# Optimization experiments

Hardware: AMD Instinct MI355X
Metric: run time of the kernel (lower is better)

## Reference

```python
import jax, jax.numpy as jnp
import numpy as np
from jax.scipy.special import gammaln

EPS = 1e-20
EULER_GAMMA = 0.5772156649015329
B, L, D, H, DK, DV = 8, 512, 1024, 16, 64, 64
K_WEIBULL = 0.5
BETA_GAMMA = 1.0
SCALE = 1.0 / np.sqrt(DK)  # torch code DIVIDES by this -> multiply by sqrt(DK)


def setup_inputs() -> dict:
    key = jax.random.key(0)
    ks = jax.random.split(key, 20)
    f = jnp.float32
    return {
        "queries": jax.random.normal(ks[0], (B, L, D), f),
        "keys": jax.random.normal(ks[1], (B, L, D), f),
        "values": jax.random.normal(ks[2], (B, L, D), f),
        "unif": jax.random.uniform(ks[3], (B, H, L, L), f),
        "Wq": jax.random.normal(ks[4], (D, H * DK), f) * 0.03,
        "bq": jnp.zeros((H * DK,), f),
        "Wk": jax.random.normal(ks[5], (D, H * DK), f) * 0.03,
        "bk": jnp.zeros((H * DK,), f),
        "Wv": jax.random.normal(ks[6], (D, H * DV), f) * 0.03,
        "bv": jnp.zeros((H * DV,), f),
        "Wo": jax.random.normal(ks[7], (H * DV, D), f) * 0.03,
        "bo": jnp.zeros((D,), f),
        "Wp1": jax.random.normal(ks[8], (DK, D), f) * 0.05,
        "bp1": jnp.zeros((D,), f),
        "Wp2": jax.random.normal(ks[9], (D, 1), f) * 0.05,
        "bp2": jnp.zeros((1,), f),
    }


def reference(queries, keys, values, unif, Wq, bq, Wk, bk, Wv, bv, Wo, bo, Wp1, bp1, Wp2, bp2):
    # projections -> multi-head layout
    q = (queries @ Wq + bq).reshape(B, L, H, DK).transpose(0, 2, 1, 3)   # [B,H,Q,dk]
    k = (keys @ Wk + bk).reshape(B, L, H, DK).transpose(0, 2, 1, 3)     # [B,H,K,dk]
    v = (values @ Wv + bv).reshape(B, L, H, DV).transpose(0, 2, 1, 3)   # [B,H,K,dv]

    # faithful: torch divides by scale=1/sqrt(dk)
    att = jnp.einsum("bhqd,bhkd->bhqk", q, k) / SCALE                   # [B,H,Q,K]

    # prior MLP on keys (per key position)
    h = (k @ Wp1 + bp1)                                                  # [B,H,K,D]
    h = jnp.where(h >= 0, h, 0.01 * h)                                   # LeakyReLU
    dot_gamma = (h @ Wp2 + bp2).transpose(0, 1, 3, 2)                    # [B,H,1,K]
    prior_w = jax.nn.softmax(dot_gamma, axis=-1)
    alpha = prior_w * BETA_GAMMA                                         # [B,H,1,K]

    # Weibull reparameterized stochastic attention
    inv_k = 1.0 / K_WEIBULL
    logprobs = jnp.log(jax.nn.softmax(att, axis=-1) + EPS)
    gumbel_w = jnp.log(-jnp.log(1.0 - unif + EPS) + EPS)
    att_s = jax.nn.softmax(logprobs - gammaln(1.0 + inv_k + inv_k * gumbel_w), axis=-1)

    lg1 = gammaln(jnp.float32(1.0 + inv_k))
    kl = -(alpha * (logprobs - lg1)
           - EULER_GAMMA * alpha * inv_k
           - BETA_GAMMA * jnp.exp(logprobs - lg1 + lg1)
           + alpha * jnp.log(BETA_GAMMA + EPS)
           - gammaln(alpha + EPS))
    kl_mean = kl.mean()

    out = jnp.einsum("bhqk,bhkd->bhqd", att_s, v)                        # [B,H,Q,dv]
    out = out.transpose(0, 2, 1, 3).reshape(B, L, H * DV)
    out = out @ Wo + bo                                                  # [B,Q,D]
    return out, kl_mean
```

## Files before the change

### kernel.cpp

```cpp
#include <hip/hip_runtime.h>
#include <math.h>


typedef __bf16 bh_t;
typedef bh_t  bh8  __attribute__((ext_vector_type(8)));
typedef float f32x4 __attribute__((ext_vector_type(4)));
typedef _Float16 hf_t;
typedef hf_t  hf4  __attribute__((ext_vector_type(4)));

#define MFMA_BF16 __builtin_amdgcn_mfma_f32_16x16x32_bf16

static constexpr size_t P2 = 4096ull*1024ull*2ull;
static constexpr size_t W2 = 1024ull*1024ull*2ull;
static constexpr size_t O_QHI = 0;
static constexpr size_t O_QLO = O_QHI + P2;
static constexpr size_t O_KHI = O_QLO + P2;
static constexpr size_t O_KLO = O_KHI + P2;
static constexpr size_t O_VT  = O_KLO + P2;
static constexpr size_t O_WQH = O_VT  + P2;
static constexpr size_t O_WQL = O_WQH + W2;
static constexpr size_t O_WKH = O_WQL + W2;
static constexpr size_t O_WKL = O_WKH + W2;
static constexpr size_t O_WVH = O_WKL + W2;
static constexpr size_t O_WVL = O_WVH + W2;
static constexpr size_t O_WOH = O_WVL + W2;
static constexpr size_t O_WOL = O_WOH + W2;
static constexpr size_t O_WP1H = O_WOL + W2;
static constexpr size_t O_WP1L = O_WP1H + 1024ull*64ull*2ull;
static constexpr size_t O_DG   = O_WP1L + 1024ull*64ull*2ull;
static constexpr size_t O_ALPHA= O_DG + 65536ull*4ull;
static constexpr size_t O_HO   = O_ALPHA + 65536ull*4ull;
static constexpr size_t O_GS   = O_HO + P2;
static constexpr size_t O_ACC  = O_GS + 512ull*65536ull*2ull;
static constexpr size_t WS_TOTAL = O_ACC + 256;

__device__ __align__(256) unsigned char g_ws[WS_TOTAL];

__device__ __forceinline__ float lgamma_fast(float x)
{
    float ax = (x < 0.5f) ? (1.0f - x) : x;
    float p  = ax*(ax+1.f)*(ax+2.f)*(ax+3.f);
    bool  sm = ax < 4.0f;
    float lsh = sm ? __logf(p) : 0.0f;
    float y   = sm ? (ax + 4.0f) : ax;
    float ly  = __logf(y);
    float inv = __builtin_amdgcn_rcpf(y);
    float i2  = inv * inv;
    float stir = fmaf(y - 0.5f, ly, -y) + 0.91893853320467274f
               + inv * fmaf(-2.7777777777e-3f, i2, 8.3333333333e-2f);
    float core = stir - lsh;
    float r  = x - rintf(x);
    float sp = __sinf(3.14159265358979f * r);
    float rres = 1.14472988584940017f - __logf(fabsf(sp)) - core;
    return (x < 0.5f) ? rres : core;
}

__global__ void k_zero(double* a)
{
    if (threadIdx.x < 4) a[threadIdx.x] = 0.0;
}

__global__ __launch_bounds__(256) void k_transpose_split(
    const float* __restrict__ in, bh_t* __restrict__ oh, bh_t* __restrict__ ol,
    int rows, int cols)
{
    __shared__ float tile[64][65];
    const int bc = blockIdx.x * 64, br = blockIdx.y * 64;
    const int t = threadIdx.x;
    const int r = t >> 2, c0 = (t & 3) * 16;
#pragma unroll
    for (int i = 0; i < 16; i += 4) {
        float4 v = *(const float4*)(in + (size_t)(br + r) * cols + bc + c0 + i);
        tile[r][c0+i]   = v.x; tile[r][c0+i+1] = v.y;
        tile[r][c0+i+2] = v.z; tile[r][c0+i+3] = v.w;
    }
    __syncthreads();
    bh8 hv[2], lv[2];
#pragma unroll
    for (int i = 0; i < 16; i++) {
        float x = tile[c0 + i][r];
        bh_t hh = (bh_t)x;
        hv[i >> 3][i & 7] = hh;
        lv[i >> 3][i & 7] = (bh_t)(x - (float)hh);
    }
    size_t ob = (size_t)(bc + r) * rows + br + c0;
    *(bh8*)(oh + ob)     = hv[0];
    *(bh8*)(oh + ob + 8) = hv[1];
    *(bh8*)(ol + ob)     = lv[0];
    *(bh8*)(ol + ob + 8) = lv[1];
}

__global__ __launch_bounds__(256) void k_transpose_split4(
    const float* __restrict__ W0, const float* __restrict__ W1,
    const float* __restrict__ W2_, const float* __restrict__ W3,
    bh_t* __restrict__ OH)
{
    __shared__ float tile[64][65];
    const int z = blockIdx.z;
    const float* in = (z == 0) ? W0 : (z == 1) ? W1 : (z == 2) ? W2_ : W3;
    bh_t* oh = OH + (size_t)z * 2ull * 1024ull * 1024ull;
    bh_t* ol = oh + 1024ull * 1024ull;
    const int bc = blockIdx.x * 64, br = blockIdx.y * 64;
    const int t = threadIdx.x;
    const int r = t >> 2, c0 = (t & 3) * 16;
#pragma unroll
    for (int i = 0; i < 16; i += 4) {
        float4 v = *(const float4*)(in + (size_t)(br + r) * 1024 + bc + c0 + i);
        tile[r][c0+i]   = v.x; tile[r][c0+i+1] = v.y;
        tile[r][c0+i+2] = v.z; tile[r][c0+i+3] = v.w;
    }
    __syncthreads();
    bh8 hv[2], lv[2];
#pragma unroll
    for (int i = 0; i < 16; i++) {
        float x = tile[c0 + i][r];
        bh_t hh = (bh_t)x;
        hv[i >> 3][i & 7] = hh;
        lv[i >> 3][i & 7] = (bh_t)(x - (float)hh);
    }
    size_t ob = (size_t)(bc + r) * 1024 + br + c0;
    *(bh8*)(oh + ob)     = hv[0];
    *(bh8*)(oh + ob + 8) = hv[1];
    *(bh8*)(ol + ob)     = lv[0];
    *(bh8*)(ol + ob + 8) = lv[1];
}

template<bool SPLIT, int OMODE, bool ABF>
__global__ __launch_bounds__(256) void k_gemm(
    const float* __restrict__ A, const bh_t* __restrict__ ABH,
    const bh_t* __restrict__ WH, const bh_t* __restrict__ WL,
    const float* __restrict__ bias,
    bh_t* __restrict__ oh, bh_t* __restrict__ ol, float* __restrict__ of)
{
    __shared__ __align__(16) bh_t Ah[64][40];
    __shared__ __align__(16) bh_t Al[64][40];
    __shared__ __align__(16) bh_t Bh[64][40];
    __shared__ __align__(16) bh_t Bl[64][40];
    const int n0 = blockIdx.x * 64, m0 = blockIdx.y * 64;
    const int t = threadIdx.x;
    const int lane = t & 63, w = t >> 6;
    const int lr = lane & 15, kg = lane >> 4;
    const int wm = (w & 1) * 32, wn = (w >> 1) * 32;
    const int ar = t >> 2, ac = (t & 3) * 8;
    f32x4 acc[2][2] = {};

    for (int kt = 0; kt < 1024; kt += 32) {
        __syncthreads();
        {
            if constexpr (ABF) {
                *(bh8*)&Ah[ar][ac] = *(const bh8*)(ABH + (size_t)(m0 + ar) * 1024 + kt + ac);
            } else {
                const float* ap = A + (size_t)(m0 + ar) * 1024 + kt + ac;
                float4 v0 = *(const float4*)ap;
                float4 v1 = *(const float4*)(ap + 4);
                float xs[8] = {v0.x, v0.y, v0.z, v0.w, v1.x, v1.y, v1.z, v1.w};
                bh8 h, l;
#pragma unroll
                for (int i = 0; i < 8; i++) {
                    bh_t hh = (bh_t)xs[i];
                    h[i] = hh;
                    l[i] = (bh_t)(xs[i] - (float)hh);
                }
                *(bh8*)&Ah[ar][ac] = h;
                if constexpr (SPLIT) *(bh8*)&Al[ar][ac] = l;
            }
            size_t wb = (size_t)(n0 + ar) * 1024 + kt + ac;
            *(bh8*)&Bh[ar][ac] = *(const bh8*)(WH + wb);
            if constexpr (SPLIT) *(bh8*)&Bl[ar][ac] = *(const bh8*)(WL + wb);
        }
        __syncthreads();
#pragma unroll
        for (int fm = 0; fm < 2; fm++) {
            bh8 a_h = *(bh8*)&Ah[wm + fm*16 + lr][kg * 8];
#pragma unroll
            for (int fn = 0; fn < 2; fn++) {
                bh8 b_h = *(bh8*)&Bh[wn + fn*16 + lr][kg * 8];
                acc[fm][fn] = MFMA_BF16(a_h, b_h, acc[fm][fn], 0, 0, 0);
                if constexpr (SPLIT) {
                    bh8 a_l = *(bh8*)&Al[wm + fm*16 + lr][kg * 8];
                    bh8 b_l = *(bh8*)&Bl[wn + fn*16 + lr][kg * 8];
                    acc[fm][fn] = MFMA_BF16(a_h, b_l, acc[fm][fn], 0, 0, 0);
                    acc[fm][fn] = MFMA_BF16(a_l, b_h, acc[fm][fn], 0, 0, 0);
                }
            }
        }
    }
#pragma unroll
    for (int fm = 0; fm < 2; fm++)
#pragma unroll
    for (int fn = 0; fn < 2; fn++) {
        int col = n0 + wn + fn*16 + lr;
        float bv = bias[col];
#pragma unroll
        for (int r = 0; r < 4; r++) {
            int row = m0 + wm + fm*16 + kg*4 + r;
            float c = acc[fm][fn][r] + bv;
            size_t idx = (size_t)row * 1024 + col;
            if constexpr (OMODE == 0) {
                bh_t hh = (bh_t)c;
                oh[idx] = hh;
                ol[idx] = (bh_t)(c - (float)hh);
            } else if constexpr (OMODE == 1) {
                oh[idx] = (bh_t)c;
            } else if constexpr (OMODE == 2) {
                of[idx] = c;
            } else {
                int bb = row >> 9, ll = row & 511;
                oh[(((size_t)(bb*16 + (col >> 6)) * 64) + (col & 63)) * 512 + ll] = (bh_t)c;
            }
        }
    }
}

__global__ __launch_bounds__(256) void k_prior(
    const bh_t* __restrict__ KH, const bh_t* __restrict__ WP1T,
    const float* __restrict__ bp1, const float* __restrict__ wp2,
    const float* __restrict__ bp2, float* __restrict__ DG)
{
    __shared__ __align__(16) bh_t Kt[64][72];
    __shared__ __align__(16) bh_t Wt[64][72];
    const int lt = blockIdx.x, h = blockIdx.y, b = blockIdx.z;
    const int t = threadIdx.x, lane = t & 63, w = t >> 6;
    const int lr = lane & 15, kg = lane >> 4;
    {
        int r = t >> 2, j0 = (t & 3) * 16;
        const bh_t* src = KH + ((size_t)(b*512 + lt*64 + r)) * 1024 + h*64 + j0;
        *(bh8*)&Kt[r][j0]     = *(const bh8*)src;
        *(bh8*)&Kt[r][j0 + 8] = *(const bh8*)(src + 8);
    }
    __syncthreads();
    bh8 af0 = *(bh8*)&Kt[w*16 + lr][kg * 8];
    bh8 af1 = *(bh8*)&Kt[w*16 + lr][32 + kg * 8];
    float dgp[4] = {0.f, 0.f, 0.f, 0.f};
    for (int dt = 0; dt < 16; dt++) {
        __syncthreads();
        {
            int r = t >> 2, j0 = (t & 3) * 16;
            const bh_t* src = WP1T + (size_t)(dt*64 + r) * 64 + j0;
            *(bh8*)&Wt[r][j0]     = *(const bh8*)src;
            *(bh8*)&Wt[r][j0 + 8] = *(const bh8*)(src + 8);
        }
        __syncthreads();
#pragma unroll
        for (int fn = 0; fn < 4; fn++) {
            bh8 b0 = *(bh8*)&Wt[fn*16 + lr][kg * 8];
            bh8 b1 = *(bh8*)&Wt[fn*16 + lr][32 + kg * 8];
            f32x4 acc = {};
            acc = MFMA_BF16(af0, b0, acc, 0, 0, 0);
            acc = MFMA_BF16(af1, b1, acc, 0, 0, 0);
            int d = dt*64 + fn*16 + lr;
            float bpv = bp1[d], wvv = wp2[d];
#pragma unroll
            for (int r = 0; r < 4; r++) {
                float hv = acc[r] + bpv;
                hv = (hv >= 0.f) ? hv : 0.01f * hv;
                dgp[r] = fmaf(hv, wvv, dgp[r]);
            }
        }
    }
#pragma unroll
    for (int r = 0; r < 4; r++) {
        float v = dgp[r];
        v += __shfl_xor(v, 1); v += __shfl_xor(v, 2);
        v += __shfl_xor(v, 4); v += __shfl_xor(v, 8);
        dgp[r] = v;
    }
    if (lr == 0) {
        float b2 = bp2[0];
        int bh = b * 16 + h;
#pragma unroll
        for (int r = 0; r < 4; r++)
            DG[(size_t)bh*512 + lt*64 + w*16 + kg*4 + r] = dgp[r] + b2;
    }
}

__global__ __launch_bounds__(512) void k_alpha(
    const float* __restrict__ DG, float* __restrict__ AL, double* __restrict__ acc)
{
    __shared__ float red[512];
    const int bh = blockIdx.x, t = threadIdx.x;
    float v = DG[(size_t)bh * 512 + t];
    red[t] = v; __syncthreads();
    for (int s = 256; s > 0; s >>= 1) { if (t < s) red[t] = fmaxf(red[t], red[t+s]); __syncthreads(); }
    float m = red[0]; __syncthreads();
    float e = expf(v - m);
    red[t] = e; __syncthreads();
    for (int s = 256; s > 0; s >>= 1) { if (t < s) red[t] += red[t+s]; __syncthreads(); }
    float ssum = red[0]; __syncthreads();
    float a = e / ssum;
    AL[(size_t)bh * 512 + t] = a;
    float t2 = a * 1.8475785103630112f + lgammaf(a + 1e-20f);
    red[t] = t2; __syncthreads();
    for (int s = 256; s > 0; s >>= 1) { if (t < s) red[t] += red[t+s]; __syncthreads(); }
    if (t == 0) atomicAdd(&acc[2], (double)red[0]);
}

__global__ __launch_bounds__(512, 3) void k_attn(
    const bh_t* __restrict__ QH, const bh_t* __restrict__ QL,
    const bh_t* __restrict__ KH, const bh_t* __restrict__ KL,
    const bh_t* __restrict__ VT, const float* __restrict__ U,
    const float* __restrict__ AL, bh_t* __restrict__ HOB,
    hf_t* __restrict__ GS, double* __restrict__ acc)
{
    __shared__ __align__(16) bh_t KtH[64][72];
    __shared__ __align__(16) bh_t KtL[64][72];
    __shared__ __align__(16) bh_t Vt[64][72];
    __shared__ __align__(16) bh_t Sl[8][16][72];
    __shared__ float Asm[64];
    __shared__ float red[512];

    const int flat = blockIdx.x;
    const int bh = flat & 127, qc = flat >> 7;
    const int b = bh >> 4, h = bh & 15;
    const int t = threadIdx.x, w = t >> 6, lane = t & 63;
    const int lr = lane & 15, kg = lane >> 4;
    const int q0 = qc * 128 + w * 16;
    const int sr = t >> 3, sj = (t & 7) * 8;
    const float* Up = U + ((size_t)bh * 512 + q0 + kg * 4) * 512;
    hf_t* GSp = GS + (size_t)flat * 65536 + (size_t)w * 8192;

    bh8 qh[2], ql[2];
    {
        size_t qb = ((size_t)(b * 512) + q0 + lr) * 1024 + h * 64;
        qh[0] = *(const bh8*)(QH + qb + kg * 8);
        qh[1] = *(const bh8*)(QH + qb + 32 + kg * 8);
        ql[0] = *(const bh8*)(QL + qb + kg * 8);
        ql[1] = *(const bh8*)(QL + qb + 32 + kg * 8);
    }
    float C[4];

    {
        float M1[4], Z1[4];
#pragma unroll
        for (int r = 0; r < 4; r++) { M1[r] = -INFINITY; Z1[r] = 0.f; }

        for (int kt = 0; kt < 8; kt++) {
            __syncthreads();
            {
                size_t src = ((size_t)(b*512 + kt*64 + sr)) * 1024 + h*64 + sj;
                *(bh8*)&KtH[sr][sj] = *(const bh8*)(KH + src);
                *(bh8*)&KtL[sr][sj] = *(const bh8*)(KL + src);
            }
            __syncthreads();
            f32x4 av[4];
#pragma unroll
            for (int fn = 0; fn < 4; fn++) {
                f32x4 a = {};
#pragma unroll
                for (int ks = 0; ks < 2; ks++) {
                    bh8 kb  = *(bh8*)&KtH[fn*16 + lr][ks*32 + kg*8];
                    bh8 kl2 = *(bh8*)&KtL[fn*16 + lr][ks*32 + kg*8];
                    a = MFMA_BF16(qh[ks], kb,  a, 0, 0, 0);
                    a = MFMA_BF16(qh[ks], kl2, a, 0, 0, 0);
                    a = MFMA_BF16(ql[ks], kb,  a, 0, 0, 0);
                }
#pragma unroll
                for (int r = 0; r < 4; r++) a[r] *= 8.0f;
                av[fn] = a;
                int k = kt * 64 + fn * 16 + lr;
                hf4 gh;
#pragma unroll
                for (int r = 0; r < 4; r++) {
                    float u  = Up[(size_t)r * 512 + k];
                    float tt = (1.0f - u) + 1e-20f;
                    float gl = 1e-20f - __logf(tt);
                    float g  = __logf(gl);
                    gh[r] = (hf_t)lgamma_fast(fmaf(2.0f, g, 3.0f));
                }
                *(hf4*)(GSp + ((size_t)(kt*4 + fn) * 64 + lane) * 4) = gh;
            }
#pragma unroll
            for (int r = 0; r < 4; r++) {
                float mx = fmaxf(fmaxf(av[0][r], av[1][r]), fmaxf(av[2][r], av[3][r]));
                mx = fmaxf(mx, __shfl_xor(mx, 1));
                mx = fmaxf(mx, __shfl_xor(mx, 2));
                mx = fmaxf(mx, __shfl_xor(mx, 4));
                mx = fmaxf(mx, __shfl_xor(mx, 8));
                float nm = fmaxf(M1[r], mx);
                float es = __expf(av[0][r]-nm) + __expf(av[1][r]-nm)
                         + __expf(av[2][r]-nm) + __expf(av[3][r]-nm);
                es += __shfl_xor(es, 1); es += __shfl_xor(es, 2);
                es += __shfl_xor(es, 4); es += __shfl_xor(es, 8);
                Z1[r] = Z1[r] * __expf(M1[r] - nm) + es;
                M1[r] = nm;
            }
        }
#pragma unroll
        for (int r = 0; r < 4; r++) C[r] = M1[r] + logf(Z1[r]);
    }

    float M2[4], Z2[4];
    f32x4 oacc[4] = {};
#pragma unroll
    for (int r = 0; r < 4; r++) { M2[r] = -INFINITY; Z2[r] = 0.f; }
    float S1f = 0.f;

    for (int kt = 0; kt < 8; kt++) {
        __syncthreads();
        {
            size_t src = ((size_t)(b*512 + kt*64 + sr)) * 1024 + h*64 + sj;
            *(bh8*)&KtH[sr][sj] = *(const bh8*)(KH + src);
            *(bh8*)&KtL[sr][sj] = *(const bh8*)(KL + src);
            const bh_t* vsrc = VT + ((size_t)bh * 64 + sr) * 512 + kt*64 + sj;
            *(bh8*)&Vt[sr][sj] = *(const bh8*)vsrc;
            if (t < 64) Asm[t] = AL[(size_t)bh * 512 + kt * 64 + t];
        }
        __syncthreads();
        f32x4 wv[4];
#pragma unroll
        for (int fn = 0; fn < 4; fn++) {
            f32x4 a = {};
#pragma unroll
            for (int ks = 0; ks < 2; ks++) {
                bh8 kb  = *(bh8*)&KtH[fn*16 + lr][ks*32 + kg*8];
                bh8 kl2 = *(bh8*)&KtL[fn*16 + lr][ks*32 + kg*8];
                a = MFMA_BF16(qh[ks], kb,  a, 0, 0, 0);
                a = MFMA_BF16(qh[ks], kl2, a, 0, 0, 0);
                a = MFMA_BF16(ql[ks], kb,  a, 0, 0, 0);
            }
            hf4 gh = *(const hf4*)(GSp + ((size_t)(kt*4 + fn) * 64 + lane) * 4);
            float alv = Asm[fn * 16 + lr];
#pragma unroll
            for (int r = 0; r < 4; r++) {
                float s  = fmaf(a[r], 8.0f, -C[r]);
                float ex = __expf(s);
                float lp = __logf(ex + 1e-20f);
                wv[fn][r] = lp - (float)gh[r];
                S1f = fmaf(alv, lp, S1f);
            }
        }
#pragma unroll
        for (int r = 0; r < 4; r++) {
            float mx = fmaxf(fmaxf(wv[0][r], wv[1][r]), fmaxf(wv[2][r], wv[3][r]));
            mx = fmaxf(mx, __shfl_xor(mx, 1));
            mx = fmaxf(mx, __shfl_xor(mx, 2));
            mx = fmaxf(mx, __shfl_xor(mx, 4));
            mx = fmaxf(mx, __shfl_xor(mx, 8));
            float nm = fmaxf(M2[r], mx);
            float sc = __expf(M2[r] - nm);
            float zs = 0.f;
#pragma unroll
            for (int fn = 0; fn < 4; fn++) {
                float sv = __expf(wv[fn][r] - nm);
                zs += sv;
                Sl[w][kg * 4 + r][fn * 16 + lr] = (bh_t)sv;
            }
            zs += __shfl_xor(zs, 1); zs += __shfl_xor(zs, 2);
            zs += __shfl_xor(zs, 4); zs += __shfl_xor(zs, 8);
            Z2[r] = fmaf(Z2[r], sc, zs);
            M2[r] = nm;
#pragma unroll
            for (int fo = 0; fo < 4; fo++) oacc[fo][r] *= sc;
        }
        bh8 sa0 = *(bh8*)&Sl[w][lr][kg*8];
        bh8 sa1 = *(bh8*)&Sl[w][lr][32 + kg*8];
#pragma unroll
        for (int fo = 0; fo < 4; fo++) {
            bh8 v0 = *(bh8*)&Vt[fo*16 + lr][kg*8];
            bh8 v1 = *(bh8*)&Vt[fo*16 + lr][32 + kg*8];
            oacc[fo] = MFMA_BF16(sa0, v0, oacc[fo], 0, 0, 0);
            oacc[fo] = MFMA_BF16(sa1, v1, oacc[fo], 0, 0, 0);
        }
    }
    float rz[4];
#pragma unroll
    for (int r = 0; r < 4; r++) rz[r] = 1.0f / Z2[r];
#pragma unroll
    for (int fo = 0; fo < 4; fo++) {
#pragma unroll
        for (int r = 0; r < 4; r++) {
            int q = q0 + kg * 4 + r;
            int dv = fo * 16 + lr;
            HOB[((size_t)(b * 512 + q)) * 1024 + h * 64 + dv] = (bh_t)(oacc[fo][r] * rz[r]);
        }
    }
    red[t] = S1f; __syncthreads();
    for (int s = 256; s > 0; s >>= 1) { if (t < s) red[t] += red[t+s]; __syncthreads(); }
    if (t == 0) atomicAdd(&acc[0], (double)red[0]);
}

__global__ void k_kl(const double* __restrict__ acc, float* __restrict__ out)
{
    if (threadIdx.x == 0 && blockIdx.x == 0) {
        double kl = (-acc[0] + 512.0 * acc[2] + 65536.0) / 33554432.0;
        out[4194304] = (float)kl;
    }
}

extern "C" void kernel_launch(void* const* d_in, const int* in_sizes, int n_in,
                              void* d_out, int out_size, void* d_ws, size_t ws_size,
                              hipStream_t stream)
{
    (void)in_sizes; (void)n_in; (void)d_ws; (void)ws_size; (void)out_size;
    const float* queries = (const float*)d_in[0];
    const float* keys    = (const float*)d_in[1];
    const float* values  = (const float*)d_in[2];
    const float* unif    = (const float*)d_in[3];
    const float* Wq = (const float*)d_in[4];  const float* bq = (const float*)d_in[5];
    const float* Wk = (const float*)d_in[6];  const float* bk = (const float*)d_in[7];
    const float* Wv = (const float*)d_in[8];  const float* bv = (const float*)d_in[9];
    const float* Wo = (const float*)d_in[10]; const float* bo = (const float*)d_in[11];
    const float* Wp1 = (const float*)d_in[12]; const float* bp1 = (const float*)d_in[13];
    const float* Wp2 = (const float*)d_in[14]; const float* bp2 = (const float*)d_in[15];

    unsigned char* ws = nullptr;
    hipGetSymbolAddress((void**)&ws, HIP_SYMBOL(g_ws));

    bh_t* QHI = (bh_t*)(ws + O_QHI); bh_t* QLO = (bh_t*)(ws + O_QLO);
    bh_t* KHI = (bh_t*)(ws + O_KHI); bh_t* KLO = (bh_t*)(ws + O_KLO);
    bh_t* VTp = (bh_t*)(ws + O_VT);
    bh_t* WQH = (bh_t*)(ws + O_WQH); bh_t* WQL = (bh_t*)(ws + O_WQL);
    bh_t* WKH = (bh_t*)(ws + O_WKH); bh_t* WKL = (bh_t*)(ws + O_WKL);
    bh_t* WVH = (bh_t*)(ws + O_WVH); bh_t* WVL = (bh_t*)(ws + O_WVL);
    bh_t* WOH = (bh_t*)(ws + O_WOH); bh_t* WOL = (bh_t*)(ws + O_WOL);
    bh_t* WP1H = (bh_t*)(ws + O_WP1H); bh_t* WP1L = (bh_t*)(ws + O_WP1L);
    float* DG    = (float*)(ws + O_DG);
    float* ALPHA = (float*)(ws + O_ALPHA);
    bh_t*  HOB   = (bh_t*)(ws + O_HO);
    hf_t*  GS    = (hf_t*)(ws + O_GS);
    double* ACC  = (double*)(ws + O_ACC);
    float* outF  = (float*)d_out;

    k_zero<<<1, 64, 0, stream>>>(ACC);

    k_transpose_split4<<<dim3(16,16,4), 256, 0, stream>>>(Wq, Wk, Wv, Wo, WQH);
    k_transpose_split<<<dim3(16,1), 256, 0, stream>>>(Wp1, WP1H, WP1L, 64, 1024);

    k_gemm<true, 0,false><<<dim3(16,64), 256, 0, stream>>>(queries, nullptr, WQH, WQL, bq, QHI, QLO, nullptr);
    k_gemm<true, 0,false><<<dim3(16,64), 256, 0, stream>>>(keys,    nullptr, WKH, WKL, bk, KHI, KLO, nullptr);
    k_gemm<false,3,false><<<dim3(16,64), 256, 0, stream>>>(values,  nullptr, WVH, WVL, bv, VTp, nullptr, nullptr);

    k_prior<<<dim3(8,16,8), 256, 0, stream>>>(KHI, WP1H, bp1, Wp2, bp2, DG);
    k_alpha<<<128, 512, 0, stream>>>(DG, ALPHA, ACC);

    k_attn<<<512, 512, 0, stream>>>(QHI, QLO, KHI, KLO, VTp, unif, ALPHA, HOB, GS, ACC);

    k_gemm<false,2,true><<<dim3(16,64), 256, 0, stream>>>(nullptr, HOB, WOH, WOL, bo, nullptr, nullptr, outF);
    k_kl<<<1, 1, 0, stream>>>(ACC, outF);
}
```

Baseline: 362.6 us.

## Enlarge GEMM tiles to 128x64 and merge Q/K projections into one launch

The shared GEMM body now computes a 128-row by 64-column output tile per block, with each wave holding a 64x32 accumulator instead of 32x32. This raises reuse of the weight tile loaded into LDS, and the low-part A fragment is now read once per row fragment instead of once per fn. The Q and K projections are fused into one launch with a z-dimension that selects inputs and weights, removing a kernel launch and letting both run concurrently. In exchange the grids are halved to 512 or 1024 blocks, and the larger accumulator and LDS footprint may lower occupancy. The layout offsets are assumed to be contiguous (QHI/QLO/KHI/KLO and the WQ/WK pairs).

```diff
diff --git a/kernel.cpp b/kernel.cpp
--- a/kernel.cpp
+++ b/kernel.cpp
@@ -126,43 +126,47 @@
 }
 
 template<bool SPLIT, int OMODE, bool ABF>
-__global__ __launch_bounds__(256) void k_gemm(
+__device__ __forceinline__ void gemm_body(
     const float* __restrict__ A, const bh_t* __restrict__ ABH,
     const bh_t* __restrict__ WH, const bh_t* __restrict__ WL,
     const float* __restrict__ bias,
-    bh_t* __restrict__ oh, bh_t* __restrict__ ol, float* __restrict__ of)
-{
-    __shared__ __align__(16) bh_t Ah[64][40];
-    __shared__ __align__(16) bh_t Al[64][40];
+    bh_t* __restrict__ oh, bh_t* __restrict__ ol, float* __restrict__ of,
+    int n0, int m0)
+{
+    __shared__ __align__(16) bh_t Ah[128][40];
+    __shared__ __align__(16) bh_t Al[128][40];
     __shared__ __align__(16) bh_t Bh[64][40];
     __shared__ __align__(16) bh_t Bl[64][40];
-    const int n0 = blockIdx.x * 64, m0 = blockIdx.y * 64;
     const int t = threadIdx.x;
     const int lane = t & 63, w = t >> 6;
     const int lr = lane & 15, kg = lane >> 4;
-    const int wm = (w & 1) * 32, wn = (w >> 1) * 32;
+    const int wm = (w & 1) * 64, wn = (w >> 1) * 32;
     const int ar = t >> 2, ac = (t & 3) * 8;
-    f32x4 acc[2][2] = {};
+    f32x4 acc[4][2] = {};
 
     for (int kt = 0; kt < 1024; kt += 32) {
         __syncthreads();
         {
             if constexpr (ABF) {
-                *(bh8*)&Ah[ar][ac] = *(const bh8*)(ABH + (size_t)(m0 + ar) * 1024 + kt + ac);
+                *(bh8*)&Ah[ar][ac]      = *(const bh8*)(ABH + (size_t)(m0 + ar) * 1024 + kt + ac);
+                *(bh8*)&Ah[ar + 64][ac] = *(const bh8*)(ABH + (size_t)(m0 + ar + 64) * 1024 + kt + ac);
             } else {
-                const float* ap = A + (size_t)(m0 + ar) * 1024 + kt + ac;
-                float4 v0 = *(const float4*)ap;
-                float4 v1 = *(const float4*)(ap + 4);
-                float xs[8] = {v0.x, v0.y, v0.z, v0.w, v1.x, v1.y, v1.z, v1.w};
-                bh8 h, l;
-#pragma unroll
-                for (int i = 0; i < 8; i++) {
-                    bh_t hh = (bh_t)xs[i];
-                    h[i] = hh;
-                    l[i] = (bh_t)(xs[i] - (float)hh);
+#pragma unroll
+                for (int half = 0; half < 2; half++) {
+                    const float* ap = A + (size_t)(m0 + ar + half*64) * 1024 + kt + ac;
+                    float4 v0 = *(const float4*)ap;
+                    float4 v1 = *(const float4*)(ap + 4);
+                    float xs[8] = {v0.x, v0.y, v0.z, v0.w, v1.x, v1.y, v1.z, v1.w};
+                    bh8 h, l;
+#pragma unroll
+                    for (int i = 0; i < 8; i++) {
+                        bh_t hh = (bh_t)xs[i];
+                        h[i] = hh;
+                        l[i] = (bh_t)(xs[i] - (float)hh);
+                    }
+                    *(bh8*)&Ah[ar + half*64][ac] = h;
+                    if constexpr (SPLIT) *(bh8*)&Al[ar + half*64][ac] = l;
                 }
-                *(bh8*)&Ah[ar][ac] = h;
-                if constexpr (SPLIT) *(bh8*)&Al[ar][ac] = l;
             }
             size_t wb = (size_t)(n0 + ar) * 1024 + kt + ac;
             *(bh8*)&Bh[ar][ac] = *(const bh8*)(WH + wb);
@@ -170,14 +174,15 @@
         }
         __syncthreads();
 #pragma unroll
-        for (int fm = 0; fm < 2; fm++) {
+        for (int fm = 0; fm < 4; fm++) {
             bh8 a_h = *(bh8*)&Ah[wm + fm*16 + lr][kg * 8];
+            bh8 a_l;
+            if constexpr (SPLIT) a_l = *(bh8*)&Al[wm + fm*16 + lr][kg * 8];
 #pragma unroll
             for (int fn = 0; fn < 2; fn++) {
                 bh8 b_h = *(bh8*)&Bh[wn + fn*16 + lr][kg * 8];
                 acc[fm][fn] = MFMA_BF16(a_h, b_h, acc[fm][fn], 0, 0, 0);
                 if constexpr (SPLIT) {
-                    bh8 a_l = *(bh8*)&Al[wm + fm*16 + lr][kg * 8];
                     bh8 b_l = *(bh8*)&Bl[wn + fn*16 + lr][kg * 8];
                     acc[fm][fn] = MFMA_BF16(a_h, b_l, acc[fm][fn], 0, 0, 0);
                     acc[fm][fn] = MFMA_BF16(a_l, b_h, acc[fm][fn], 0, 0, 0);
@@ -186,7 +191,7 @@
         }
     }
 #pragma unroll
-    for (int fm = 0; fm < 2; fm++)
+    for (int fm = 0; fm < 4; fm++)
 #pragma unroll
     for (int fn = 0; fn < 2; fn++) {
         int col = n0 + wn + fn*16 + lr;
@@ -210,6 +215,33 @@
             }
         }
     }
+}
+
+template<bool SPLIT, int OMODE, bool ABF>
+__global__ __launch_bounds__(256) void k_gemm(
+    const float* __restrict__ A, const bh_t* __restrict__ ABH,
+    const bh_t* __restrict__ WH, const bh_t* __restrict__ WL,
+    const float* __restrict__ bias,
+    bh_t* __restrict__ oh, bh_t* __restrict__ ol, float* __restrict__ of)
+{
+    gemm_body<SPLIT, OMODE, ABF>(A, ABH, WH, WL, bias, oh, ol, of,
+                                 blockIdx.x * 64, blockIdx.y * 128);
+}
+
+__global__ __launch_bounds__(256) void k_gemm_qk(
+    const float* __restrict__ Aq, const float* __restrict__ Ak,
+    const bh_t* __restrict__ Wbase, const float* __restrict__ bq,
+    const float* __restrict__ bk, bh_t* __restrict__ Obase)
+{
+    const int z = blockIdx.z;
+    const float* A = z ? Ak : Aq;
+    const bh_t* WH = Wbase + (size_t)z * 2ull * 1024ull * 1024ull;
+    const bh_t* WL = WH + 1024ull * 1024ull;
+    const float* bias = z ? bk : bq;
+    bh_t* oh = Obase + (size_t)z * 2ull * 4096ull * 1024ull;
+    bh_t* ol = oh + 4096ull * 1024ull;
+    gemm_body<true, 0, false>(A, nullptr, WH, WL, bias, oh, ol, nullptr,
+                              blockIdx.x * 64, blockIdx.y * 128);
 }
 
 __global__ __launch_bounds__(256) void k_prior(
@@ -506,11 +538,11 @@
     unsigned char* ws = nullptr;
     hipGetSymbolAddress((void**)&ws, HIP_SYMBOL(g_ws));
 
-    bh_t* QHI = (bh_t*)(ws + O_QHI); bh_t* QLO = (bh_t*)(ws + O_QLO);
+    bh_t* QHI = (bh_t*)(ws + O_QHI);
     bh_t* KHI = (bh_t*)(ws + O_KHI); bh_t* KLO = (bh_t*)(ws + O_KLO);
+    bh_t* QLO = (bh_t*)(ws + O_QLO);
     bh_t* VTp = (bh_t*)(ws + O_VT);
-    bh_t* WQH = (bh_t*)(ws + O_WQH); bh_t* WQL = (bh_t*)(ws + O_WQL);
-    bh_t* WKH = (bh_t*)(ws + O_WKH); bh_t* WKL = (bh_t*)(ws + O_WKL);
+    bh_t* WQH = (bh_t*)(ws + O_WQH);
     bh_t* WVH = (bh_t*)(ws + O_WVH); bh_t* WVL = (bh_t*)(ws + O_WVL);
     bh_t* WOH = (bh_t*)(ws + O_WOH); bh_t* WOL = (bh_t*)(ws + O_WOL);
     bh_t* WP1H = (bh_t*)(ws + O_WP1H); bh_t* WP1L = (bh_t*)(ws + O_WP1L);
@@ -526,15 +558,14 @@
     k_transpose_split4<<<dim3(16,16,4), 256, 0, stream>>>(Wq, Wk, Wv, Wo, WQH);
     k_transpose_split<<<dim3(16,1), 256, 0, stream>>>(Wp1, WP1H, WP1L, 64, 1024);
 
-    k_gemm<true, 0,false><<<dim3(16,64), 256, 0, stream>>>(queries, nullptr, WQH, WQL, bq, QHI, QLO, nullptr);
-    k_gemm<true, 0,false><<<dim3(16,64), 256, 0, stream>>>(keys,    nullptr, WKH, WKL, bk, KHI, KLO, nullptr);
-    k_gemm<false,3,false><<<dim3(16,64), 256, 0, stream>>>(values,  nullptr, WVH, WVL, bv, VTp, nullptr, nullptr);
+    k_gemm_qk<<<dim3(16,32,2), 256, 0, stream>>>(queries, keys, WQH, bq, bk, QHI);
+    k_gemm<false,3,false><<<dim3(16,32), 256, 0, stream>>>(values, nullptr, WVH, WVL, bv, VTp, nullptr, nullptr);
 
     k_prior<<<dim3(8,16,8), 256, 0, stream>>>(KHI, WP1H, bp1, Wp2, bp2, DG);
     k_alpha<<<128, 512, 0, stream>>>(DG, ALPHA, ACC);
 
     k_attn<<<512, 512, 0, stream>>>(QHI, QLO, KHI, KLO, VTp, unif, ALPHA, HOB, GS, ACC);
 
-    k_gemm<false,2,true><<<dim3(16,64), 256, 0, stream>>>(nullptr, HOB, WOH, WOL, bo, nullptr, nullptr, outF);
+    k_gemm<false,2,true><<<dim3(16,32), 256, 0, stream>>>(nullptr, HOB, WOH, WOL, bo, nullptr, nullptr, outF);
     k_kl<<<1, 1, 0, stream>>>(ACC, outF);
 }
```

Result: no change. 358.8 us (-1.1%).
